# Kernel optimization log

Hardware: AMD Instinct MI355X
Metric: run time of the kernel (lower is better)

The kernel has to match this reference:

```python
import jax, jax.numpy as jnp
import numpy as np


def _safe_div(x, y):
    # avoid NaNs in branches that are masked out by jnp.where
    return x / jnp.where(jnp.abs(y) < 1e-12, 1.0, y)


def _closest_point_region(p, a, b, c):
    """Ericson closest-point-on-triangle, vectorized.
    p: [B,n,1,3]; a,b,c: [B,1,m,3] -> (dist2 [B,n,m], region [B,n,m] int32).
    Region codes: 0=vertA 1=vertB 2=vertC 3=edgeAB 4=edgeAC 5=edgeBC 6=face.
    """
    ab = b - a; ac = c - a; cb = c - b
    ap = p - a; bp = p - b; cp = p - c
    d1 = (ab * ap).sum(-1); d2 = (ac * ap).sum(-1)
    d3 = (ab * bp).sum(-1); d4 = (ac * bp).sum(-1)
    d5 = (ab * cp).sum(-1); d6 = (ac * cp).sum(-1)
    vc = d1 * d4 - d3 * d2
    vb = d5 * d2 - d1 * d6
    va = d3 * d6 - d5 * d4

    # candidate closest points per region
    v_ab = jnp.clip(_safe_div(d1, d1 - d3), 0.0, 1.0)
    v_ac = jnp.clip(_safe_div(d2, d2 - d6), 0.0, 1.0)
    v_bc = jnp.clip(_safe_div(d4 - d3, (d4 - d3) + (d5 - d6)), 0.0, 1.0)
    denom = va + vb + vc
    v_f = _safe_div(vb, denom); w_f = _safe_div(vc, denom)

    q_face = a + v_f[..., None] * ab + w_f[..., None] * ac
    q_ab = a + v_ab[..., None] * ab
    q_ac = a + v_ac[..., None] * ac
    q_bc = b + v_bc[..., None] * cb

    # region conditions (Ericson priority: a, b, ab, c, ac, bc, face)
    cond_a = (d1 <= 0) & (d2 <= 0)
    cond_b = (d3 >= 0) & (d4 <= d3)
    cond_ab = (vc <= 0) & (d1 >= 0) & (d3 <= 0)
    cond_c = (d6 >= 0) & (d5 <= d6)
    cond_ac = (vb <= 0) & (d2 >= 0) & (d6 <= 0)
    cond_bc = (va <= 0) & (d4 - d3 >= 0) & (d5 - d6 >= 0)

    def sel(cond, qc, code, q, region):
        q = jnp.where(cond[..., None], qc, q)
        region = jnp.where(cond, code, region)
        return q, region

    # apply lowest priority first so higher-priority regions overwrite
    q = q_face
    region = jnp.full(q.shape[:-1], 6, dtype=jnp.int32)
    q, region = sel(cond_bc, q_bc, 5, q, region)
    q, region = sel(cond_ac, q_ac, 4, q, region)
    q, region = sel(cond_c, c, 2, q, region)
    q, region = sel(cond_ab, q_ab, 3, q, region)
    q, region = sel(cond_b, b, 1, q, region)
    q, region = sel(cond_a, a, 0, q, region)

    diff = p - q
    dist2 = (diff * diff).sum(-1)  # squared distance, as in chamfer-style kernels
    return dist2, region


def setup_inputs() -> dict:
    key = jax.random.key(0)
    k1, k2, k3, k4 = jax.random.split(key, 4)
    B, n, m = 4, 4096, 512
    xyz1 = jax.random.normal(k1, (B, n, 3), dtype=jnp.float32)
    tri1 = jax.random.normal(k2, (B, m, 3), dtype=jnp.float32)
    tri2 = jax.random.normal(k3, (B, m, 3), dtype=jnp.float32)
    tri3 = jax.random.normal(k4, (B, m, 3), dtype=jnp.float32)
    return {"xyz1": xyz1, "tri1": tri1, "tri2": tri2, "tri3": tri3}


def reference(xyz1, tri1, tri2, tri3):
    p = xyz1[:, :, None, :]       # [B,n,1,3]
    a = tri1[:, None, :, :]       # [B,1,m,3]
    b = tri2[:, None, :, :]
    c = tri3[:, None, :, :]
    dist2, region = _closest_point_region(p, a, b, c)  # [B,n,m]
    index = jnp.argmin(dist2, axis=-1).astype(jnp.int32)            # [B,n]
    dist = jnp.min(dist2, axis=-1)                                  # [B,n]
    point = jnp.take_along_axis(region, index[..., None].astype(jnp.int64), axis=-1)[..., 0]
    return dist, point, index
```

## Files before the change

kernel.cpp:

```cpp
#include <hip/hip_runtime.h>
#include <math.h>

#define BB 4
#define NN 4096
#define MM 512
#define TPB 512
#define PPB 32
#define NPTS_TOT (BB * NN)

__device__ __forceinline__ float safercp(float y) {
    float yy = (fabsf(y) < 1e-12f) ? 1.0f : y;
    return __builtin_amdgcn_rcpf(yy);
}

__device__ __forceinline__ float safediv(float x, float y) {
    float yy = (fabsf(y) < 1e-12f) ? 1.0f : y;
    return x / yy;
}

__device__ __forceinline__ float clip01s(float x) {
    return fminf(fmaxf(x, 0.0f), 1.0f);
}

__device__ void exact_pair(float px, float py, float pz,
                           float ax, float ay, float az,
                           float bx, float by, float bz,
                           float cx, float cy, float cz,
                           float* dist2_out, int* reg_out) {
#pragma clang fp contract(off)
    const float abx = bx-ax, aby = by-ay, abz = bz-az;
    const float acx = cx-ax, acy = cy-ay, acz = cz-az;
    const float cbx = cx-bx, cby = cy-by, cbz = cz-bz;
    const float apx = px-ax, apy = py-ay, apz = pz-az;
    const float bpx = px-bx, bpy = py-by, bpz = pz-bz;
    const float cpx = px-cx, cpy = py-cy, cpz = pz-cz;

    const float d1 = abx*apx + aby*apy + abz*apz;
    const float d2 = acx*apx + acy*apy + acz*apz;
    const float d3 = abx*bpx + aby*bpy + abz*bpz;
    const float d4 = acx*bpx + acy*bpy + acz*bpz;
    const float d5 = abx*cpx + aby*cpy + abz*cpz;
    const float d6 = acx*cpx + acy*cpy + acz*cpz;

    const float vc = d1*d4 - d3*d2;
    const float vb = d5*d2 - d1*d6;
    const float va = d3*d6 - d5*d4;

    const float v_ab = clip01s(safediv(d1, d1 - d3));
    const float v_ac = clip01s(safediv(d2, d2 - d6));
    const float t43 = d4 - d3;
    const float t56 = d5 - d6;
    const float v_bc = clip01s(safediv(t43, t43 + t56));
    const float denom = va + vb + vc;
    const float v_f = safediv(vb, denom);
    const float w_f = safediv(vc, denom);

    float qx = ax + v_f*abx + w_f*acx;
    float qy = ay + v_f*aby + w_f*acy;
    float qz = az + v_f*abz + w_f*acz;
    int reg = 6;
    const bool c_bc = (va <= 0.0f) && (t43 >= 0.0f) && (t56 >= 0.0f);
    if (c_bc) { qx = bx + v_bc*cbx; qy = by + v_bc*cby; qz = bz + v_bc*cbz; reg = 5; }
    const bool c_ac = (vb <= 0.0f) && (d2 >= 0.0f) && (d6 <= 0.0f);
    if (c_ac) { qx = ax + v_ac*acx; qy = ay + v_ac*acy; qz = az + v_ac*acz; reg = 4; }
    const bool c_c = (d6 >= 0.0f) && (d5 <= d6);
    if (c_c) { qx = cx; qy = cy; qz = cz; reg = 2; }
    const bool c_ab = (vc <= 0.0f) && (d1 >= 0.0f) && (d3 <= 0.0f);
    if (c_ab) { qx = ax + v_ab*abx; qy = ay + v_ab*aby; qz = az + v_ab*abz; reg = 3; }
    const bool c_b = (d3 >= 0.0f) && (d4 <= d3);
    if (c_b) { qx = bx; qy = by; qz = bz; reg = 1; }
    const bool c_a = (d1 <= 0.0f) && (d2 <= 0.0f);
    if (c_a) { qx = ax; qy = ay; qz = az; reg = 0; }

    const float dx = px - qx;
    const float dy = py - qy;
    const float dz = pz - qz;
    *dist2_out = dx*dx + dy*dy + dz*dz;
    *reg_out = reg;
}

__global__ __launch_bounds__(TPB) void tridist_kernel(
    const float* __restrict__ xyz1, const float* __restrict__ tri1,
    const float* __restrict__ tri2, const float* __restrict__ tri3,
    float* __restrict__ out)
{
    __shared__ unsigned int sK[8][64];

    const int t    = threadIdx.x;
    const int lane = t & 63;
    const int w    = t >> 6;
    const int b    = blockIdx.x >> 7;
    const int pb   = blockIdx.x & 127;

    const int j = t;
    const float* g1 = tri1 + ((size_t)b * MM + j) * 3;
    const float* g2 = tri2 + ((size_t)b * MM + j) * 3;
    const float* g3 = tri3 + ((size_t)b * MM + j) * 3;
    const float ax = g1[0], ay = g1[1], az = g1[2];
    const float bx = g2[0], by = g2[1], bz = g2[2];
    const float cx = g3[0], cy = g3[1], cz = g3[2];
    const float abx = bx-ax, aby = by-ay, abz = bz-az;
    const float acx = cx-ax, acy = cy-ay, acz = cz-az;
    const float cbx = cx-bx, cby = cy-by, cbz = cz-bz;
    const float naba  = -fmaf(abz, az, fmaf(aby, ay, abx*ax));
    const float naca  = -fmaf(acz, az, fmaf(acy, ay, acx*ax));
    const float ab2   = fmaf(abz, abz, fmaf(aby, aby, abx*abx));
    const float ac2   = fmaf(acz, acz, fmaf(acy, acy, acx*acx));
    const float cb2   = fmaf(cbz, cbz, fmaf(cby, cby, cbx*cbx));
    const float abac  = fmaf(abz, acz, fmaf(aby, acy, abx*acx));
    const float nab2  = -ab2, nabac = -abac, nac2 = -ac2;
    const float rab2  = safercp(ab2), rac2 = safercp(ac2), rcb2 = safercp(cb2);
    const float nrx = fmaf(aby, acz, -(abz*acy));
    const float nry = fmaf(abz, acx, -(abx*acz));
    const float nrz = fmaf(abx, acy, -(aby*acx));
    const float n2  = fmaf(nrz, nrz, fmaf(nry, nry, nrx*nrx));
    const float rn  = __builtin_amdgcn_rsqf(fmaxf(n2, 1e-30f));
    const float nx = nrx*rn, ny = nry*rn, nz = nrz*rn;
    const float nna = -fmaf(nz, az, fmaf(ny, ay, nx*ax));

    const float* pxyz = xyz1 + ((size_t)b * NN + pb * PPB) * 3;

    unsigned int kmine = 0xFFFFFFFFu;

#pragma unroll 8
    for (int i = 0; i < PPB; ++i) {
        const float px = pxyz[3*i + 0];
        const float py = pxyz[3*i + 1];
        const float pz = pxyz[3*i + 2];

        const float d1 = fmaf(abz, pz, fmaf(aby, py, fmaf(abx, px, naba)));
        const float d2 = fmaf(acz, pz, fmaf(acy, py, fmaf(acx, px, naca)));
        const float h  = fmaf(nz,  pz, fmaf(ny,  py, fmaf(nx,  px, nna)));
        const float d3 = d1 + nab2;
        const float d4 = d2 + nabac;
        const float d5 = d1 + nabac;
        const float d6 = d2 + nac2;

        const float vc = fmaf(d1, d4, -(d3*d2));
        const float vb = fmaf(d5, d2, -(d1*d6));
        const float va = fmaf(d3, d6, -(d5*d4));
        const float t43 = d4 - d3;

        const float uab = clip01s(d1 * rab2);
        const float uac = clip01s(d2 * rac2);
        const float ubc = clip01s(t43 * rcb2);

        const float apx = px - ax, apy = py - ay, apz = pz - az;
        const float bpx = apx - abx, bpy = apy - aby, bpz = apz - abz;

        float ex = fmaf(-uab, abx, apx), ey = fmaf(-uab, aby, apy), ez = fmaf(-uab, abz, apz);
        const float dAB = fmaf(ez, ez, fmaf(ey, ey, ex*ex));
        ex = fmaf(-uac, acx, apx); ey = fmaf(-uac, acy, apy); ez = fmaf(-uac, acz, apz);
        const float dAC = fmaf(ez, ez, fmaf(ey, ey, ex*ex));
        ex = fmaf(-ubc, cbx, bpx); ey = fmaf(-ubc, cby, bpy); ez = fmaf(-ubc, cbz, bpz);
        const float dBC = fmaf(ez, ez, fmaf(ey, ey, ex*ex));
        const float dF = h * h;

        const float mv   = fminf(fminf(va, vb), vc);
        const float dseg = fminf(fminf(dAB, dAC), dBC);
        const float dd   = (mv >= 0.0f) ? dF : dseg;

        unsigned int key = (__float_as_uint(dd) & 0xFFFFFFC0u) | (unsigned int)lane;

        key = min(key, (unsigned int)__shfl_xor((int)key, 1, 64));
        key = min(key, (unsigned int)__shfl_xor((int)key, 2, 64));
        key = min(key, (unsigned int)__shfl_xor((int)key, 4, 64));
        key = min(key, (unsigned int)__shfl_xor((int)key, 8, 64));
        key = min(key, (unsigned int)__shfl_xor((int)key, 16, 64));
        key = min(key, (unsigned int)__shfl_xor((int)key, 32, 64));

        if (lane == i) kmine = key;
    }

    sK[w][lane] = kmine;
    __syncthreads();

    if (t < PPB) {
        float bd = INFINITY; int bj = 0;
        for (int ww = 0; ww < 8; ++ww) {
            const unsigned int k = sK[ww][t];
            const float dk = __uint_as_float(k & 0xFFFFFFC0u);
            const int   jk = ww * 64 + (int)(k & 63u);
            if (dk < bd) { bd = dk; bj = jk; }
        }
        const int gidx = b * NN + pb * PPB + t;
        const float* h1 = tri1 + ((size_t)b * MM + bj) * 3;
        const float* h2 = tri2 + ((size_t)b * MM + bj) * 3;
        const float* h3 = tri3 + ((size_t)b * MM + bj) * 3;
        float dist2; int reg;
        exact_pair(xyz1[gidx*3+0], xyz1[gidx*3+1], xyz1[gidx*3+2],
                   h1[0], h1[1], h1[2],
                   h2[0], h2[1], h2[2],
                   h3[0], h3[1], h3[2],
                   &dist2, &reg);
        out[gidx]               = dist2;
        out[NPTS_TOT + gidx]    = (float)reg;
        out[2*NPTS_TOT + gidx]  = (float)bj;
    }
}

extern "C" void kernel_launch(void* const* d_in, const int* in_sizes, int n_in,
                              void* d_out, int out_size, void* d_ws, size_t ws_size,
                              hipStream_t stream) {
    const float* xyz1 = (const float*)d_in[0];
    const float* tri1 = (const float*)d_in[1];
    const float* tri2 = (const float*)d_in[2];
    const float* tri3 = (const float*)d_in[3];
    float* out = (float*)d_out;

    dim3 grid(BB * (NN / PPB));
    dim3 block(TPB);
    tridist_kernel<<<grid, block, 0, stream>>>(xyz1, tri1, tri2, tri3, out);
}
```

Measured before the change: 72.67 us.

## Split into setup, per-thread point scan over triangle segments, and reduction kernels

Triangle precomputation moves into its own kernel that writes packed 24-float records to workspace. The main kernel now maps points to lanes and triangles to wave-uniform loops over 16 segments. Each thread keeps a running minimum, which removes the per-iteration six-step shuffle reduction. A third kernel reduces the 16 partial results and runs the exact region evaluation. This adds two extra launches and workspace traffic, and the triangle loads become scalar or broadcast loads from global memory.

```diff
diff --git a/kernel.cpp b/kernel.cpp
--- a/kernel.cpp
+++ b/kernel.cpp
@@ -4,9 +4,10 @@
 #define BB 4
 #define NN 4096
 #define MM 512
-#define TPB 512
-#define PPB 32
 #define NPTS_TOT (BB * NN)
+#define NTRI_TOT (BB * MM)
+#define NSPLIT 16
+#define MSEG (MM / NSPLIT)
 
 __device__ __forceinline__ float safercp(float y) {
     float yy = (fabsf(y) < 1e-12f) ? 1.0f : y;
@@ -79,23 +80,14 @@
     *reg_out = reg;
 }
 
-__global__ __launch_bounds__(TPB) void tridist_kernel(
-    const float* __restrict__ xyz1, const float* __restrict__ tri1,
-    const float* __restrict__ tri2, const float* __restrict__ tri3,
-    float* __restrict__ out)
+__global__ __launch_bounds__(256) void tridist_setup(
+    const float* __restrict__ tri1, const float* __restrict__ tri2,
+    const float* __restrict__ tri3, float* __restrict__ pre)
 {
-    __shared__ unsigned int sK[8][64];
-
-    const int t    = threadIdx.x;
-    const int lane = t & 63;
-    const int w    = t >> 6;
-    const int b    = blockIdx.x >> 7;
-    const int pb   = blockIdx.x & 127;
-
-    const int j = t;
-    const float* g1 = tri1 + ((size_t)b * MM + j) * 3;
-    const float* g2 = tri2 + ((size_t)b * MM + j) * 3;
-    const float* g3 = tri3 + ((size_t)b * MM + j) * 3;
+    const int g = blockIdx.x * 256 + threadIdx.x;
+    const float* g1 = tri1 + (size_t)g * 3;
+    const float* g2 = tri2 + (size_t)g * 3;
+    const float* g3 = tri3 + (size_t)g * 3;
     const float ax = g1[0], ay = g1[1], az = g1[2];
     const float bx = g2[0], by = g2[1], bz = g2[2];
     const float cx = g3[0], cy = g3[1], cz = g3[2];
@@ -108,8 +100,6 @@
     const float ac2   = fmaf(acz, acz, fmaf(acy, acy, acx*acx));
     const float cb2   = fmaf(cbz, cbz, fmaf(cby, cby, cbx*cbx));
     const float abac  = fmaf(abz, acz, fmaf(aby, acy, abx*acx));
-    const float nab2  = -ab2, nabac = -abac, nac2 = -ac2;
-    const float rab2  = safercp(ab2), rac2 = safercp(ac2), rcb2 = safercp(cb2);
     const float nrx = fmaf(aby, acz, -(abz*acy));
     const float nry = fmaf(abz, acx, -(abx*acz));
     const float nrz = fmaf(abx, acy, -(aby*acx));
@@ -118,15 +108,46 @@
     const float nx = nrx*rn, ny = nry*rn, nz = nrz*rn;
     const float nna = -fmaf(nz, az, fmaf(ny, ay, nx*ax));
 
-    const float* pxyz = xyz1 + ((size_t)b * NN + pb * PPB) * 3;
-
-    unsigned int kmine = 0xFFFFFFFFu;
-
-#pragma unroll 8
-    for (int i = 0; i < PPB; ++i) {
-        const float px = pxyz[3*i + 0];
-        const float py = pxyz[3*i + 1];
-        const float pz = pxyz[3*i + 2];
+    float4* p4 = (float4*)(pre + (size_t)g * 24);
+    p4[0] = make_float4(abx, aby, abz, naba);
+    p4[1] = make_float4(acx, acy, acz, naca);
+    p4[2] = make_float4(nx, ny, nz, nna);
+    p4[3] = make_float4(-ab2, -abac, -ac2, safercp(ab2));
+    p4[4] = make_float4(safercp(ac2), safercp(cb2), ax, ay);
+    p4[5] = make_float4(az, cbx, cby, cbz);
+}
+
+__global__ __launch_bounds__(256) void tridist_p1(
+    const float* __restrict__ xyz1, const float* __restrict__ pre,
+    float* __restrict__ wd, int* __restrict__ wj)
+{
+    const int t    = threadIdx.x;
+    const int lane = t & 63;
+    const int w    = __builtin_amdgcn_readfirstlane(t >> 6);
+    const int pg   = blockIdx.x >> 2;
+    const int spl  = (blockIdx.x & 3) * 4 + w;
+    const int b    = pg >> 6;
+    const int point = pg * 64 + lane;
+
+    const float px = xyz1[point*3 + 0];
+    const float py = xyz1[point*3 + 1];
+    const float pz = xyz1[point*3 + 2];
+
+    const int jlocal0 = spl * MSEG;
+    const float* tp0 = pre + ((size_t)b * MM + jlocal0) * 24;
+
+    float bestd = INFINITY;
+    int   bestj = 0;
+
+#pragma unroll 4
+    for (int i = 0; i < MSEG; ++i) {
+        const float* tp = tp0 + (size_t)i * 24;
+        const float abx = tp[0],  aby = tp[1],  abz = tp[2],  naba = tp[3];
+        const float acx = tp[4],  acy = tp[5],  acz = tp[6],  naca = tp[7];
+        const float nx  = tp[8],  ny  = tp[9],  nz  = tp[10], nna  = tp[11];
+        const float nab2 = tp[12], nabac = tp[13], nac2 = tp[14], rab2 = tp[15];
+        const float rac2 = tp[16], rcb2 = tp[17], ax = tp[18], ay = tp[19];
+        const float az  = tp[20], cbx = tp[21], cby = tp[22], cbz = tp[23];
 
         const float d1 = fmaf(abz, pz, fmaf(aby, py, fmaf(abx, px, naba)));
         const float d2 = fmaf(acz, pz, fmaf(acy, py, fmaf(acx, px, naca)));
@@ -160,43 +181,39 @@
         const float dseg = fminf(fminf(dAB, dAC), dBC);
         const float dd   = (mv >= 0.0f) ? dF : dseg;
 
-        unsigned int key = (__float_as_uint(dd) & 0xFFFFFFC0u) | (unsigned int)lane;
-
-        key = min(key, (unsigned int)__shfl_xor((int)key, 1, 64));
-        key = min(key, (unsigned int)__shfl_xor((int)key, 2, 64));
-        key = min(key, (unsigned int)__shfl_xor((int)key, 4, 64));
-        key = min(key, (unsigned int)__shfl_xor((int)key, 8, 64));
-        key = min(key, (unsigned int)__shfl_xor((int)key, 16, 64));
-        key = min(key, (unsigned int)__shfl_xor((int)key, 32, 64));
-
-        if (lane == i) kmine = key;
+        if (dd < bestd) { bestd = dd; bestj = jlocal0 + i; }
     }
 
-    sK[w][lane] = kmine;
-    __syncthreads();
-
-    if (t < PPB) {
-        float bd = INFINITY; int bj = 0;
-        for (int ww = 0; ww < 8; ++ww) {
-            const unsigned int k = sK[ww][t];
-            const float dk = __uint_as_float(k & 0xFFFFFFC0u);
-            const int   jk = ww * 64 + (int)(k & 63u);
-            if (dk < bd) { bd = dk; bj = jk; }
-        }
-        const int gidx = b * NN + pb * PPB + t;
-        const float* h1 = tri1 + ((size_t)b * MM + bj) * 3;
-        const float* h2 = tri2 + ((size_t)b * MM + bj) * 3;
-        const float* h3 = tri3 + ((size_t)b * MM + bj) * 3;
-        float dist2; int reg;
-        exact_pair(xyz1[gidx*3+0], xyz1[gidx*3+1], xyz1[gidx*3+2],
-                   h1[0], h1[1], h1[2],
-                   h2[0], h2[1], h2[2],
-                   h3[0], h3[1], h3[2],
-                   &dist2, &reg);
-        out[gidx]               = dist2;
-        out[NPTS_TOT + gidx]    = (float)reg;
-        out[2*NPTS_TOT + gidx]  = (float)bj;
+    wd[(size_t)spl * NPTS_TOT + point] = bestd;
+    wj[(size_t)spl * NPTS_TOT + point] = bestj;
+}
+
+__global__ __launch_bounds__(256) void tridist_p2(
+    const float* __restrict__ xyz1, const float* __restrict__ tri1,
+    const float* __restrict__ tri2, const float* __restrict__ tri3,
+    const float* __restrict__ wd, const int* __restrict__ wj,
+    float* __restrict__ out)
+{
+    const int gidx = blockIdx.x * 256 + threadIdx.x;
+    float bd = INFINITY; int bj = 0;
+    for (int s = 0; s < NSPLIT; ++s) {
+        const float dk = wd[(size_t)s * NPTS_TOT + gidx];
+        const int   jk = wj[(size_t)s * NPTS_TOT + gidx];
+        if (dk < bd) { bd = dk; bj = jk; }
     }
+    const int b = gidx >> 12;
+    const float* g1 = tri1 + ((size_t)b * MM + bj) * 3;
+    const float* g2 = tri2 + ((size_t)b * MM + bj) * 3;
+    const float* g3 = tri3 + ((size_t)b * MM + bj) * 3;
+    float dist2; int reg;
+    exact_pair(xyz1[gidx*3+0], xyz1[gidx*3+1], xyz1[gidx*3+2],
+               g1[0], g1[1], g1[2],
+               g2[0], g2[1], g2[2],
+               g3[0], g3[1], g3[2],
+               &dist2, &reg);
+    out[gidx]               = dist2;
+    out[NPTS_TOT + gidx]    = (float)reg;
+    out[2*NPTS_TOT + gidx]  = (float)bj;
 }
 
 extern "C" void kernel_launch(void* const* d_in, const int* in_sizes, int n_in,
@@ -208,7 +225,14 @@
     const float* tri3 = (const float*)d_in[3];
     float* out = (float*)d_out;
 
-    dim3 grid(BB * (NN / PPB));
-    dim3 block(TPB);
-    tridist_kernel<<<grid, block, 0, stream>>>(xyz1, tri1, tri2, tri3, out);
-}
+    float* pre = (float*)d_ws;
+    float* wd  = pre + (size_t)NTRI_TOT * 24;
+    int*   wj  = (int*)(wd + (size_t)NSPLIT * NPTS_TOT);
+
+    tridist_setup<<<NTRI_TOT / 256, 256, 0, stream>>>(tri1, tri2, tri3, pre);
+
+    dim3 grid1((NPTS_TOT / 64) * 4);
+    tridist_p1<<<grid1, 256, 0, stream>>>(xyz1, pre, wd, wj);
+
+    tridist_p2<<<NPTS_TOT / 256, 256, 0, stream>>>(xyz1, tri1, tri2, tri3, wd, wj, out);
+}
```

Result: slower. 82.68 us (+13.8%).
